# Kernel tuning notes

Hardware: AMD Instinct MI355X
Metric: run time of the kernel (lower is better)

## Reference

```python
import jax, jax.numpy as jnp
import numpy as np

B, S, D, N, H = 2, 1024, 1024, 16, 64
R = 2 * S          # max relative length
EPS = 1e-9
INF = 1000000.0
SHIFT = 1          # q_len == context_len branch


def _forward(query, key, value, r, cls_mask, Wq, Wk, bk, Wv, bv, Wo, bo,
             r_w_bias, r_r_bias, r_kernel, r_s_bias, seg_embed, ln_gamma, ln_beta,
             token_type_mat, attention_mask):
    scale = 1.0 / np.sqrt(H).astype(np.float32)
    q = (query @ Wq).reshape(B, S, N, H) * scale          # [b,s,n,h]
    k = (key @ Wk + bk).reshape(B, S, N, H)
    v = (value @ Wv + bv).reshape(B, S, N, H)

    # content score
    content = jnp.einsum('binh,bjnh->bnij', q + r_w_bias * scale, k)

    # relative positional score with shift-gather trick
    r_head = jnp.einsum('td,dnh->tnh', r, r_kernel)        # [2S,n,h]
    pos = jnp.einsum('binh,tnh->bnit', q + r_r_bias * scale, r_head)  # [b,n,s,2S]
    pos = pos.reshape(B, N, R, S)[:, :, SHIFT:, :].reshape(B, N, S, R - SHIFT)[..., :S]
    pos = pos * cls_mask

    # token-type (segment) score: seg_embed[0]=diff, seg_embed[1]=same
    tt_bias = jnp.einsum('binh,snh->bnis', q + r_s_bias * scale, seg_embed)  # [b,n,s,2]
    diff, same = tt_bias[..., :1], tt_bias[..., 1:]
    tt = jnp.where(token_type_mat[:, None], same, diff) * cls_mask           # [b,n,s,s]

    mask = attention_mask.astype(jnp.float32)[:, None, None]                 # [b,1,1,s]
    attn_score = content + pos + tt - INF * (1.0 - mask)
    attn_prob = jax.nn.softmax(attn_score, axis=-1)

    attn_vec = jnp.einsum('bnij,bjnh->binh', attn_prob, v).reshape(B, S, N * H)
    attn_out = attn_vec @ Wo + bo

    x = query + attn_out
    mu = jnp.mean(x, axis=-1, keepdims=True)
    var = jnp.mean(jnp.square(x - mu), axis=-1, keepdims=True)
    return (x - mu) * jax.lax.rsqrt(var + EPS) * ln_gamma + ln_beta


def setup_inputs() -> dict:
    rng = jax.random.key(0)
    ks = jax.random.split(rng, 16)
    init = 0.02
    inp = {
        'query': jax.random.normal(ks[0], (B, S, D), jnp.float32),
        'key':   jax.random.normal(ks[1], (B, S, D), jnp.float32),
        'value': jax.random.normal(ks[2], (B, S, D), jnp.float32),
        'r':     jax.random.normal(ks[3], (R, D), jnp.float32),
        'cls_mask': jnp.ones((S, S), jnp.float32),
        'Wq': jax.random.normal(ks[4], (D, N * H), jnp.float32) * init,
        'Wk': jax.random.normal(ks[5], (D, N * H), jnp.float32) * init,
        'bk': jnp.zeros((N * H,), jnp.float32),
        'Wv': jax.random.normal(ks[6], (D, N * H), jnp.float32) * init,
        'bv': jnp.zeros((N * H,), jnp.float32),
        'Wo': jax.random.normal(ks[7], (N * H, D), jnp.float32) * init,
        'bo': jnp.zeros((D,), jnp.float32),
        'r_w_bias': jax.random.normal(ks[8], (N, H), jnp.float32) * init,
        'r_r_bias': jax.random.normal(ks[9], (N, H), jnp.float32) * init,
        'r_kernel': jax.random.normal(ks[10], (D, N, H), jnp.float32) * init,
        'r_s_bias': jax.random.normal(ks[11], (N, H), jnp.float32) * init,
        'seg_embed': jax.random.normal(ks[12], (2, N, H), jnp.float32) * init,
        'ln_gamma': jnp.ones((D,), jnp.float32),
        'ln_beta': jnp.zeros((D,), jnp.float32),
        'token_type_mat': jax.random.randint(ks[13], (B, S, S), 0, 2).astype(bool),
        'attention_mask': jax.random.randint(ks[14], (B, S), 0, 2).astype(jnp.int32),
    }
    return inp


def reference(query, key, value, r, cls_mask, Wq, Wk, bk, Wv, bv, Wo, bo,
              r_w_bias, r_r_bias, r_kernel, r_s_bias, seg_embed, ln_gamma, ln_beta,
              token_type_mat, attention_mask):
    return _forward(query, key, value, r, cls_mask, Wq, Wk, bk, Wv, bv, Wo, bo,
                    r_w_bias, r_r_bias, r_kernel, r_s_bias, seg_embed, ln_gamma, ln_beta,
                    token_type_mat, attention_mask)
```

## Files before the change

### kernel.cpp

```cpp
#include <hip/hip_runtime.h>

#define S_ 1024

typedef short short8 __attribute__((ext_vector_type(8)));
typedef float floatx4 __attribute__((ext_vector_type(4)));

static __device__ __forceinline__ float b2f(ushort u) {
    union { float f; unsigned int i; } x; x.i = ((unsigned int)u) << 16; return x.f;
}
static __device__ __forceinline__ ushort f2b(float f) {
    union { float f; unsigned int i; } x; x.f = f;
    unsigned int r = (x.i + 0x7fffu + ((x.i >> 16) & 1u)) >> 16;
    return (ushort)r;
}
static __device__ __forceinline__ void async_copy16(ushort* lds, const ushort* g) {
    __builtin_amdgcn_global_load_lds((const __attribute__((address_space(1))) void*)g,
                                     (__attribute__((address_space(3))) void*)lds, 16, 0, 0);
}

struct PreArgs {
    const float* csrc[4]; ushort* cdst[4];
    const float* tsrc[5]; ushort* tdst[5];
    const int* ttm; unsigned long long* ttb;
    const int* am;  unsigned long long* amb;
};
__global__ __launch_bounds__(256) void pre_kernel(PreArgs a) {
    int z = blockIdx.z, tid = threadIdx.x;
    if (z < 4) {
        const float* s = a.csrc[z];
        ushort* d = a.cdst[z];
        size_t idx = ((size_t)blockIdx.x * 256 + tid) * 8;
        float4 f0 = *(const float4*)&s[idx];
        float4 f1 = *(const float4*)&s[idx + 4];
        alignas(16) ushort u[8] = {f2b(f0.x), f2b(f0.y), f2b(f0.z), f2b(f0.w),
                                   f2b(f1.x), f2b(f1.y), f2b(f1.z), f2b(f1.w)};
        *(uint4*)&d[idx] = *(uint4*)u;
    } else if (z < 9) {
        const float* src = a.tsrc[z - 4];
        ushort* dst = a.tdst[z - 4];
        __shared__ float tile[32][33];
        int bx = (blockIdx.x & 31) * 32, by = (blockIdx.x >> 5) * 32;
        int tx = tid & 31, ty = tid >> 5;
#pragma unroll
        for (int i = 0; i < 32; i += 8)
            tile[ty + i][tx] = src[(size_t)(by + ty + i) * 1024 + bx + tx];
        __syncthreads();
#pragma unroll
        for (int i = 0; i < 32; i += 8)
            dst[(size_t)(bx + ty + i) * 1024 + by + tx] = f2b(tile[tx][ty + i]);
    } else {
        int w = tid >> 6, lane = tid & 63;
        int waveid = blockIdx.x * 4 + w;
#pragma unroll
        for (int t = 0; t < 8; t++) {
            int word = waveid * 8 + t;
            unsigned long long m = __ballot(a.ttm[(size_t)word * 64 + lane] != 0);
            if (lane == 0) a.ttb[word] = m;
        }
        if (blockIdx.x == 0 && w == 0) {
            for (int t = 0; t < 32; t++) {
                unsigned long long m = __ballot(a.am[(size_t)t * 64 + lane] != 0);
                if (lane == 0) a.amb[t] = m;
            }
        }
    }
}

struct ProjArgs {
    const ushort* A[4];
    const ushort* BT[4];
    const float* bias[4];
    ushort* C[4];
    float scale[4];
};
__global__ __launch_bounds__(256, 2) void gemm_proj(ProjArgs args) {
    int z = blockIdx.z;
    const ushort* A = args.A[z];
    const ushort* BT = args.BT[z];
    const float* bias = args.bias[z];
    ushort* C = args.C[z];
    float scale = args.scale[z];

    __shared__ alignas(16) ushort As[128 * 64];
    __shared__ alignas(16) ushort Bs[128 * 64];
    int n0 = blockIdx.x * 128, m0 = blockIdx.y * 128;
    int tid = threadIdx.x, lane = tid & 63, w = tid >> 6;
    int wm = (w >> 1) * 64, wn = (w & 1) * 64;
    int li = lane & 15, q4 = lane >> 4;
    floatx4 acc[4][4] = {};
    for (int k0 = 0; k0 < 1024; k0 += 64) {
        __syncthreads();
#pragma unroll
        for (int t = 0; t < 4; t++) {
            int c = 4 * w + t;
            const ushort* ga = &A[(size_t)(m0 + 8 * c + (lane >> 3)) * 1024 + k0 + 8 * (lane & 7)];
            async_copy16(&As[c * 512 + lane * 8], ga);
            const ushort* gb = &BT[(size_t)(n0 + 8 * c + (lane >> 3)) * 1024 + k0 + 8 * (lane & 7)];
            async_copy16(&Bs[c * 512 + lane * 8], gb);
        }
        __syncthreads();
        short8 af[2][4], bf[2][4];
#pragma unroll
        for (int kk = 0; kk < 2; kk++) {
#pragma unroll
            for (int ms = 0; ms < 4; ms++)
                af[kk][ms] = *(const short8*)&As[(size_t)(wm + 16 * ms + li) * 64 + 32 * kk + 8 * q4];
#pragma unroll
            for (int ns = 0; ns < 4; ns++)
                bf[kk][ns] = *(const short8*)&Bs[(size_t)(wn + 16 * ns + li) * 64 + 32 * kk + 8 * q4];
        }
#pragma unroll
        for (int kk = 0; kk < 2; kk++)
#pragma unroll
            for (int ms = 0; ms < 4; ms++)
#pragma unroll
                for (int ns = 0; ns < 4; ns++)
                    acc[ms][ns] = __builtin_amdgcn_mfma_f32_16x16x32_bf16(af[kk][ms], bf[kk][ns],
                                                                          acc[ms][ns], 0, 0, 0);
    }
#pragma unroll
    for (int ns = 0; ns < 4; ns++) {
        int col = n0 + wn + 16 * ns + li;
        float bv = bias ? bias[col] : 0.f;
#pragma unroll
        for (int ms = 0; ms < 4; ms++)
#pragma unroll
            for (int rg = 0; rg < 4; rg++) {
                int row = m0 + wm + 16 * ms + 4 * q4 + rg;
                C[(size_t)row * 1024 + col] = f2b(acc[ms][ns][rg] * scale + bv);
            }
    }
}

__global__ __launch_bounds__(256, 2) void gemm_out(const ushort* __restrict__ A,
                                                   const ushort* __restrict__ BT,
                                                   const float* __restrict__ bias,
                                                   const float* __restrict__ resid,
                                                   float* __restrict__ X) {
    __shared__ alignas(16) ushort As[64 * 64];
    __shared__ alignas(16) ushort Bs[64 * 64];
    int n0 = blockIdx.x * 64, m0 = blockIdx.y * 64;
    int tid = threadIdx.x, lane = tid & 63, w = tid >> 6;
    int wm = (w >> 1) * 32, wn = (w & 1) * 32;
    int li = lane & 15, q4 = lane >> 4;
    floatx4 acc[2][2] = {};
    for (int k0 = 0; k0 < 1024; k0 += 64) {
        __syncthreads();
#pragma unroll
        for (int t = 0; t < 2; t++) {
            int c = 2 * w + t;
            const ushort* ga = &A[(size_t)(m0 + 8 * c + (lane >> 3)) * 1024 + k0 + 8 * (lane & 7)];
            async_copy16(&As[c * 512 + lane * 8], ga);
            const ushort* gb = &BT[(size_t)(n0 + 8 * c + (lane >> 3)) * 1024 + k0 + 8 * (lane & 7)];
            async_copy16(&Bs[c * 512 + lane * 8], gb);
        }
        __syncthreads();
        short8 af[2][2], bf[2][2];
#pragma unroll
        for (int kk = 0; kk < 2; kk++) {
#pragma unroll
            for (int ms = 0; ms < 2; ms++)
                af[kk][ms] = *(const short8*)&As[(size_t)(wm + 16 * ms + li) * 64 + 32 * kk + 8 * q4];
#pragma unroll
            for (int ns = 0; ns < 2; ns++)
                bf[kk][ns] = *(const short8*)&Bs[(size_t)(wn + 16 * ns + li) * 64 + 32 * kk + 8 * q4];
        }
#pragma unroll
        for (int kk = 0; kk < 2; kk++)
#pragma unroll
            for (int ms = 0; ms < 2; ms++)
#pragma unroll
                for (int ns = 0; ns < 2; ns++)
                    acc[ms][ns] = __builtin_amdgcn_mfma_f32_16x16x32_bf16(af[kk][ms], bf[kk][ns],
                                                                          acc[ms][ns], 0, 0, 0);
    }
#pragma unroll
    for (int ns = 0; ns < 2; ns++) {
        int col = n0 + wn + 16 * ns + li;
        float bv = bias[col];
#pragma unroll
        for (int ms = 0; ms < 2; ms++)
#pragma unroll
            for (int rg = 0; rg < 4; rg++) {
                int row = m0 + wm + 16 * ms + 4 * q4 + rg;
                X[(size_t)row * 1024 + col] = acc[ms][ns][rg] + bv + resid[(size_t)row * 1024 + col];
            }
    }
}

__global__ __launch_bounds__(256, 3) void attn_kernel(
    const ushort* __restrict__ qg, const ushort* __restrict__ kg,
    const ushort* __restrict__ vg, const ushort* __restrict__ rh,
    const float* __restrict__ rwb, const float* __restrict__ rrb,
    const float* __restrict__ rsb, const float* __restrict__ seg,
    const unsigned long long* __restrict__ ttb, const unsigned long long* __restrict__ amb,
    ushort* __restrict__ av) {
    __shared__ alignas(16) ushort kt[64][72];
    __shared__ alignas(16) ushort vt[64][72];
    __shared__ alignas(16) ushort rwin[128][72];
    __shared__ alignas(16) ushort pb[4][16][72];
    __shared__ float ttd[64], tts[64];

    int i0 = blockIdx.x * 64, n = blockIdx.y, b = blockIdx.z;
    int tid = threadIdx.x, lane = tid & 63, w = tid >> 6;
    int li = lane & 15, q4 = lane >> 4;
    const float SC = 0.125f;

    {
        int r = tid >> 2, hs = (tid & 3) * 16;
        const ushort* qp = &qg[(size_t)(b * S_ + i0 + r) * 1024 + n * 64 + hs];
        alignas(16) ushort tmp[16];
        *(uint4*)&tmp[0] = *(const uint4*)&qp[0];
        *(uint4*)&tmp[8] = *(const uint4*)&qp[8];
        float d = 0.f, s = 0.f;
#pragma unroll
        for (int e = 0; e < 16; e++) {
            float qv = b2f(tmp[e]);
            int h = n * 64 + hs + e;
            rwin[r][hs + e] = f2b(qv + rwb[h] * SC);
            rwin[64 + r][hs + e] = f2b(qv + rrb[h] * SC);
            float qs = qv + rsb[h] * SC;
            d += qs * seg[h];
            s += qs * seg[1024 + h];
        }
        d += __shfl_xor(d, 1, 64); d += __shfl_xor(d, 2, 64);
        s += __shfl_xor(s, 1, 64); s += __shfl_xor(s, 2, 64);
        if ((tid & 3) == 0) { ttd[r] = d; tts[r] = s; }
    }
    __syncthreads();

    short8 aw0 = *(const short8*)&rwin[16 * w + li][8 * q4];
    short8 aw1 = *(const short8*)&rwin[16 * w + li][32 + 8 * q4];
    short8 ar0 = *(const short8*)&rwin[64 + 16 * w + li][8 * q4];
    short8 ar1 = *(const short8*)&rwin[64 + 16 * w + li][32 + 8 * q4];
    float ttd_l[4], tts_l[4];
#pragma unroll
    for (int r = 0; r < 4; r++) { ttd_l[r] = ttd[16 * w + 4 * q4 + r]; tts_l[r] = tts[16 * w + 4 * q4 + r]; }

    floatx4 o[4] = {};
    float l_i[4] = {0.f, 0.f, 0.f, 0.f};
    const int woff = 48 - 16 * w;

    for (int j0 = 0; j0 < 1024; j0 += 64) {
        __syncthreads();
        {
            int r = tid >> 2, hs = (tid & 3) * 16;
            const ushort* kp = &kg[(size_t)(b * S_ + j0 + r) * 1024 + n * 64 + hs];
            *(uint4*)&kt[r][hs] = *(const uint4*)&kp[0];
            *(uint4*)&kt[r][hs + 8] = *(const uint4*)&kp[8];
        }
        {
            int g8 = tid >> 5, jp = tid & 31;
            const ushort* vp = &vg[(size_t)(b * S_ + j0 + 2 * jp) * 1024 + n * 64 + 8 * g8];
            uint4 va = *(const uint4*)vp;
            uint4 vb2 = *(const uint4*)(vp + 1024);
            alignas(16) ushort au[8], bu[8];
            *(uint4*)au = va; *(uint4*)bu = vb2;
#pragma unroll
            for (int e = 0; e < 8; e++) {
                unsigned int val = (unsigned int)au[e] | ((unsigned int)bu[e] << 16);
                *(unsigned int*)&vt[8 * g8 + e][2 * jp] = val;
            }
        }
        {
            int r = tid >> 1, hs = (tid & 1) * 32;
            int t = 1024 + j0 - i0 - 63 + r;
            if (t > 2047) t = 2047;
            const ushort* rp = &rh[(size_t)t * 1024 + n * 64 + hs];
            *(uint4*)&rwin[r][hs] = *(const uint4*)&rp[0];
            *(uint4*)&rwin[r][hs + 8] = *(const uint4*)&rp[8];
            *(uint4*)&rwin[r][hs + 16] = *(const uint4*)&rp[16];
            *(uint4*)&rwin[r][hs + 24] = *(const uint4*)&rp[24];
        }
        int wj = j0 >> 6;
        unsigned long long ambw = amb[b * 16 + wj];
        unsigned long long tb[4];
#pragma unroll
        for (int r = 0; r < 4; r++)
            tb[r] = ttb[((size_t)(b * S_) + i0 + 16 * w + 4 * q4 + r) * 16 + wj];
        __syncthreads();

        floatx4 cs[4] = {};
#pragma unroll
        for (int s = 0; s < 4; s++) {
            short8 b0 = *(const short8*)&kt[16 * s + li][8 * q4];
            short8 b1 = *(const short8*)&kt[16 * s + li][32 + 8 * q4];
            cs[s] = __builtin_amdgcn_mfma_f32_16x16x32_bf16(aw0, b0, cs[s], 0, 0, 0);
            cs[s] = __builtin_amdgcn_mfma_f32_16x16x32_bf16(aw1, b1, cs[s], 0, 0, 0);
        }
        floatx4 pz[5] = {};
#pragma unroll
        for (int s5 = 0; s5 < 5; s5++) {
            short8 b0 = *(const short8*)&rwin[woff + 16 * s5 + li][8 * q4];
            short8 b1 = *(const short8*)&rwin[woff + 16 * s5 + li][32 + 8 * q4];
            pz[s5] = __builtin_amdgcn_mfma_f32_16x16x32_bf16(ar0, b0, pz[s5], 0, 0, 0);
            pz[s5] = __builtin_amdgcn_mfma_f32_16x16x32_bf16(ar1, b1, pz[s5], 0, 0, 0);
        }

        float p[4][4];
#pragma unroll
        for (int r = 0; r < 4; r++) {
            int delta = 15 - 4 * q4 - r;
            float psum = 0.f;
#pragma unroll
            for (int s = 0; s < 4; s++) {
                int c = 16 * s + li + delta;
                int srcl = (lane & 48) | (c & 15);
                float va = __shfl(pz[s][r], srcl, 64);
                float vb = __shfl(pz[s + 1][r], srcl, 64);
                float posv = ((c >> 4) == s) ? va : vb;
                float ttv = ((tb[r] >> (16 * s + li)) & 1) ? tts_l[r] : ttd_l[r];
                float mbv = ((ambw >> (16 * s + li)) & 1) ? 0.f : -1e6f;
                float sc = cs[s][r] + posv + ttv + mbv;
                p[r][s] = __expf(sc);
                psum += p[r][s];
            }
#pragma unroll
            for (int off = 8; off >= 1; off >>= 1) psum += __shfl_xor(psum, off, 64);
            l_i[r] += psum;
        }
#pragma unroll
        for (int r = 0; r < 4; r++)
#pragma unroll
            for (int s = 0; s < 4; s++) pb[w][4 * q4 + r][16 * s + li] = f2b(p[r][s]);
#pragma unroll
        for (int ka = 0; ka < 2; ka++) {
            short8 ap = *(const short8*)&pb[w][li][32 * ka + 8 * q4];
#pragma unroll
            for (int hsub = 0; hsub < 4; hsub++) {
                short8 bv = *(const short8*)&vt[16 * hsub + li][32 * ka + 8 * q4];
                o[hsub] = __builtin_amdgcn_mfma_f32_16x16x32_bf16(ap, bv, o[hsub], 0, 0, 0);
            }
        }
    }
#pragma unroll
    for (int hsub = 0; hsub < 4; hsub++)
#pragma unroll
        for (int r = 0; r < 4; r++) {
            int i = i0 + 16 * w + 4 * q4 + r;
            int h = 16 * hsub + li;
            av[(size_t)(b * S_ + i) * 1024 + n * 64 + h] = f2b(o[hsub][r] / l_i[r]);
        }
}

__global__ __launch_bounds__(256) void ln_kernel(const float* __restrict__ X,
                                                 const float* __restrict__ gamma,
                                                 const float* __restrict__ beta,
                                                 float* __restrict__ out) {
    int row = blockIdx.x, tid = threadIdx.x;
    float4 v = *(const float4*)&X[(size_t)row * 1024 + tid * 4];
    float sum = v.x + v.y + v.z + v.w;
    float sq = v.x * v.x + v.y * v.y + v.z * v.z + v.w * v.w;
#pragma unroll
    for (int off = 32; off >= 1; off >>= 1) {
        sum += __shfl_xor(sum, off, 64);
        sq += __shfl_xor(sq, off, 64);
    }
    __shared__ float rs[4], rq[4];
    int w = tid >> 6;
    if ((tid & 63) == 0) { rs[w] = sum; rq[w] = sq; }
    __syncthreads();
    sum = rs[0] + rs[1] + rs[2] + rs[3];
    sq = rq[0] + rq[1] + rq[2] + rq[3];
    float mu = sum * (1.f / 1024.f);
    float var = sq * (1.f / 1024.f) - mu * mu;
    float rstd = rsqrtf(fmaxf(var, 0.f) + 1e-9f);
    float4 g = *(const float4*)&gamma[tid * 4];
    float4 be = *(const float4*)&beta[tid * 4];
    float4 o;
    o.x = (v.x - mu) * rstd * g.x + be.x;
    o.y = (v.y - mu) * rstd * g.y + be.y;
    o.z = (v.z - mu) * rstd * g.z + be.z;
    o.w = (v.w - mu) * rstd * g.w + be.w;
    *(float4*)&out[(size_t)row * 1024 + tid * 4] = o;
}

extern "C" void kernel_launch(void* const* d_in, const int* in_sizes, int n_in,
                              void* d_out, int out_size, void* d_ws, size_t ws_size,
                              hipStream_t stream) {
    const float* query = (const float*)d_in[0];
    const float* key   = (const float*)d_in[1];
    const float* value = (const float*)d_in[2];
    const float* r     = (const float*)d_in[3];
    const float* Wq  = (const float*)d_in[5];
    const float* Wk  = (const float*)d_in[6];
    const float* bk  = (const float*)d_in[7];
    const float* Wv  = (const float*)d_in[8];
    const float* bv  = (const float*)d_in[9];
    const float* Wo  = (const float*)d_in[10];
    const float* bo  = (const float*)d_in[11];
    const float* rwb = (const float*)d_in[12];
    const float* rrb = (const float*)d_in[13];
    const float* rk  = (const float*)d_in[14];
    const float* rsb = (const float*)d_in[15];
    const float* seg = (const float*)d_in[16];
    const float* gamma = (const float*)d_in[17];
    const float* beta  = (const float*)d_in[18];
    const int* ttm = (const int*)d_in[19];
    const int* am  = (const int*)d_in[20];
    float* out = (float*)d_out;

    char* ws = (char*)d_ws;
    const size_t MB = (size_t)1 << 20;
    ushort* WqT = (ushort*)(ws + 0 * MB);
    ushort* WkT = (ushort*)(ws + 2 * MB);
    ushort* WvT = (ushort*)(ws + 4 * MB);
    ushort* rkT = (ushort*)(ws + 6 * MB);
    ushort* WoT = (ushort*)(ws + 8 * MB);
    ushort* qf  = (ushort*)(ws + 10 * MB);
    ushort* kf  = (ushort*)(ws + 14 * MB);
    ushort* vf  = (ushort*)(ws + 18 * MB);
    ushort* qb  = (ushort*)(ws + 22 * MB);
    ushort* kb  = (ushort*)(ws + 26 * MB);
    ushort* vb  = (ushort*)(ws + 30 * MB);
    unsigned long long* ttb = (unsigned long long*)(ws + 34 * MB);
    unsigned long long* amb = (unsigned long long*)(ws + 34 * MB + 512 * 1024);
    float*  X   = (float*)(ws + 10 * MB);
    ushort* rf  = (ushort*)d_out;
    ushort* avb = (ushort*)d_out;
    ushort* rhb = (ushort*)((char*)d_out + 4 * MB);

    PreArgs pr;
    pr.csrc[0] = query; pr.csrc[1] = key; pr.csrc[2] = value; pr.csrc[3] = r;
    pr.cdst[0] = qf; pr.cdst[1] = kf; pr.cdst[2] = vf; pr.cdst[3] = rf;
    pr.tsrc[0] = Wq; pr.tsrc[1] = Wk; pr.tsrc[2] = Wv; pr.tsrc[3] = rk; pr.tsrc[4] = Wo;
    pr.tdst[0] = WqT; pr.tdst[1] = WkT; pr.tdst[2] = WvT; pr.tdst[3] = rkT; pr.tdst[4] = WoT;
    pr.ttm = ttm; pr.ttb = ttb; pr.am = am; pr.amb = amb;
    pre_kernel<<<dim3(1024, 1, 10), 256, 0, stream>>>(pr);

    ProjArgs pa;
    pa.A[0] = qf; pa.BT[0] = WqT; pa.bias[0] = nullptr; pa.C[0] = qb;  pa.scale[0] = 0.125f;
    pa.A[1] = kf; pa.BT[1] = WkT; pa.bias[1] = bk;      pa.C[1] = kb;  pa.scale[1] = 1.0f;
    pa.A[2] = vf; pa.BT[2] = WvT; pa.bias[2] = bv;      pa.C[2] = vb;  pa.scale[2] = 1.0f;
    pa.A[3] = rf; pa.BT[3] = rkT; pa.bias[3] = nullptr; pa.C[3] = rhb; pa.scale[3] = 1.0f;
    gemm_proj<<<dim3(8, 16, 4), 256, 0, stream>>>(pa);

    attn_kernel<<<dim3(16, 16, 2), 256, 0, stream>>>(qb, kb, vb, rhb, rwb, rrb, rsb, seg,
                                                     ttb, amb, avb);

    gemm_out<<<dim3(16, 32), 256, 0, stream>>>(avb, WoT, bo, query, X);
    ln_kernel<<<2048, 256, 0, stream>>>(X, gamma, beta, out);
}
```

Measured before the change: 251.5 us.

## Halve GEMM K-tile, dedupe positional shuffles, defer row-sum reduction

```diff
diff --git a/kernel.cpp b/kernel.cpp
--- a/kernel.cpp
+++ b/kernel.cpp
@@ -81,42 +81,37 @@
     ushort* C = args.C[z];
     float scale = args.scale[z];
 
-    __shared__ alignas(16) ushort As[128 * 64];
-    __shared__ alignas(16) ushort Bs[128 * 64];
+    __shared__ alignas(16) ushort As[128 * 32];
+    __shared__ alignas(16) ushort Bs[128 * 32];
     int n0 = blockIdx.x * 128, m0 = blockIdx.y * 128;
     int tid = threadIdx.x, lane = tid & 63, w = tid >> 6;
     int wm = (w >> 1) * 64, wn = (w & 1) * 64;
     int li = lane & 15, q4 = lane >> 4;
     floatx4 acc[4][4] = {};
-    for (int k0 = 0; k0 < 1024; k0 += 64) {
-        __syncthreads();
-#pragma unroll
-        for (int t = 0; t < 4; t++) {
-            int c = 4 * w + t;
-            const ushort* ga = &A[(size_t)(m0 + 8 * c + (lane >> 3)) * 1024 + k0 + 8 * (lane & 7)];
+    for (int k0 = 0; k0 < 1024; k0 += 32) {
+        __syncthreads();
+#pragma unroll
+        for (int t = 0; t < 2; t++) {
+            int c = 2 * w + t;
+            const ushort* ga = &A[(size_t)(m0 + 16 * c + (lane >> 2)) * 1024 + k0 + 8 * (lane & 3)];
             async_copy16(&As[c * 512 + lane * 8], ga);
-            const ushort* gb = &BT[(size_t)(n0 + 8 * c + (lane >> 3)) * 1024 + k0 + 8 * (lane & 7)];
+            const ushort* gb = &BT[(size_t)(n0 + 16 * c + (lane >> 2)) * 1024 + k0 + 8 * (lane & 3)];
             async_copy16(&Bs[c * 512 + lane * 8], gb);
         }
         __syncthreads();
-        short8 af[2][4], bf[2][4];
-#pragma unroll
-        for (int kk = 0; kk < 2; kk++) {
-#pragma unroll
-            for (int ms = 0; ms < 4; ms++)
-                af[kk][ms] = *(const short8*)&As[(size_t)(wm + 16 * ms + li) * 64 + 32 * kk + 8 * q4];
+        short8 af[4], bf[4];
+#pragma unroll
+        for (int ms = 0; ms < 4; ms++)
+            af[ms] = *(const short8*)&As[(wm + 16 * ms + li) * 32 + 8 * q4];
+#pragma unroll
+        for (int ns = 0; ns < 4; ns++)
+            bf[ns] = *(const short8*)&Bs[(wn + 16 * ns + li) * 32 + 8 * q4];
+#pragma unroll
+        for (int ms = 0; ms < 4; ms++)
 #pragma unroll
             for (int ns = 0; ns < 4; ns++)
-                bf[kk][ns] = *(const short8*)&Bs[(size_t)(wn + 16 * ns + li) * 64 + 32 * kk + 8 * q4];
-        }
-#pragma unroll
-        for (int kk = 0; kk < 2; kk++)
-#pragma unroll
-            for (int ms = 0; ms < 4; ms++)
-#pragma unroll
-                for (int ns = 0; ns < 4; ns++)
-                    acc[ms][ns] = __builtin_amdgcn_mfma_f32_16x16x32_bf16(af[kk][ms], bf[kk][ns],
-                                                                          acc[ms][ns], 0, 0, 0);
+                acc[ms][ns] = __builtin_amdgcn_mfma_f32_16x16x32_bf16(af[ms], bf[ns],
+                                                                      acc[ms][ns], 0, 0, 0);
     }
 #pragma unroll
     for (int ns = 0; ns < 4; ns++) {
@@ -137,42 +132,36 @@
                                                    const float* __restrict__ bias,
                                                    const float* __restrict__ resid,
                                                    float* __restrict__ X) {
-    __shared__ alignas(16) ushort As[64 * 64];
-    __shared__ alignas(16) ushort Bs[64 * 64];
+    __shared__ alignas(16) ushort As[64 * 32];
+    __shared__ alignas(16) ushort Bs[64 * 32];
     int n0 = blockIdx.x * 64, m0 = blockIdx.y * 64;
     int tid = threadIdx.x, lane = tid & 63, w = tid >> 6;
     int wm = (w >> 1) * 32, wn = (w & 1) * 32;
     int li = lane & 15, q4 = lane >> 4;
     floatx4 acc[2][2] = {};
-    for (int k0 = 0; k0 < 1024; k0 += 64) {
-        __syncthreads();
-#pragma unroll
-        for (int t = 0; t < 2; t++) {
-            int c = 2 * w + t;
-            const ushort* ga = &A[(size_t)(m0 + 8 * c + (lane >> 3)) * 1024 + k0 + 8 * (lane & 7)];
+    for (int k0 = 0; k0 < 1024; k0 += 32) {
+        __syncthreads();
+        {
+            int c = w;
+            const ushort* ga = &A[(size_t)(m0 + 16 * c + (lane >> 2)) * 1024 + k0 + 8 * (lane & 3)];
             async_copy16(&As[c * 512 + lane * 8], ga);
-            const ushort* gb = &BT[(size_t)(n0 + 8 * c + (lane >> 3)) * 1024 + k0 + 8 * (lane & 7)];
+            const ushort* gb = &BT[(size_t)(n0 + 16 * c + (lane >> 2)) * 1024 + k0 + 8 * (lane & 3)];
             async_copy16(&Bs[c * 512 + lane * 8], gb);
         }
         __syncthreads();
-        short8 af[2][2], bf[2][2];
-#pragma unroll
-        for (int kk = 0; kk < 2; kk++) {
-#pragma unroll
-            for (int ms = 0; ms < 2; ms++)
-                af[kk][ms] = *(const short8*)&As[(size_t)(wm + 16 * ms + li) * 64 + 32 * kk + 8 * q4];
+        short8 af[2], bf[2];
+#pragma unroll
+        for (int ms = 0; ms < 2; ms++)
+            af[ms] = *(const short8*)&As[(wm + 16 * ms + li) * 32 + 8 * q4];
+#pragma unroll
+        for (int ns = 0; ns < 2; ns++)
+            bf[ns] = *(const short8*)&Bs[(wn + 16 * ns + li) * 32 + 8 * q4];
+#pragma unroll
+        for (int ms = 0; ms < 2; ms++)
 #pragma unroll
             for (int ns = 0; ns < 2; ns++)
-                bf[kk][ns] = *(const short8*)&Bs[(size_t)(wn + 16 * ns + li) * 64 + 32 * kk + 8 * q4];
-        }
-#pragma unroll
-        for (int kk = 0; kk < 2; kk++)
-#pragma unroll
-            for (int ms = 0; ms < 2; ms++)
-#pragma unroll
-                for (int ns = 0; ns < 2; ns++)
-                    acc[ms][ns] = __builtin_amdgcn_mfma_f32_16x16x32_bf16(af[kk][ms], bf[kk][ns],
-                                                                          acc[ms][ns], 0, 0, 0);
+                acc[ms][ns] = __builtin_amdgcn_mfma_f32_16x16x32_bf16(af[ms], bf[ns],
+                                                                      acc[ms][ns], 0, 0, 0);
     }
 #pragma unroll
     for (int ns = 0; ns < 2; ns++) {
@@ -301,23 +290,21 @@
 #pragma unroll
         for (int r = 0; r < 4; r++) {
             int delta = 15 - 4 * q4 - r;
-            float psum = 0.f;
+            int c0 = li + delta;
+            int srcl = (lane & 48) | (c0 & 15);
+            float bp[5];
+#pragma unroll
+            for (int t = 0; t < 5; t++) bp[t] = __shfl(pz[t][r], srcl, 64);
+            bool lo = c0 < 16;
 #pragma unroll
             for (int s = 0; s < 4; s++) {
-                int c = 16 * s + li + delta;
-                int srcl = (lane & 48) | (c & 15);
-                float va = __shfl(pz[s][r], srcl, 64);
-                float vb = __shfl(pz[s + 1][r], srcl, 64);
-                float posv = ((c >> 4) == s) ? va : vb;
+                float posv = lo ? bp[s] : bp[s + 1];
                 float ttv = ((tb[r] >> (16 * s + li)) & 1) ? tts_l[r] : ttd_l[r];
                 float mbv = ((ambw >> (16 * s + li)) & 1) ? 0.f : -1e6f;
                 float sc = cs[s][r] + posv + ttv + mbv;
                 p[r][s] = __expf(sc);
-                psum += p[r][s];
-            }
-#pragma unroll
-            for (int off = 8; off >= 1; off >>= 1) psum += __shfl_xor(psum, off, 64);
-            l_i[r] += psum;
+                l_i[r] += p[r][s];
+            }
         }
 #pragma unroll
         for (int r = 0; r < 4; r++)
@@ -333,6 +320,10 @@
             }
         }
     }
+#pragma unroll
+    for (int r = 0; r < 4; r++)
+#pragma unroll
+        for (int off = 8; off >= 1; off >>= 1) l_i[r] += __shfl_xor(l_i[r], off, 64);
 #pragma unroll
     for (int hsub = 0; hsub < 4; hsub++)
 #pragma unroll
```

Measured after the change: 282.1 us. 1.12x slower.
